# Optimization experiments

Measured on AMD Instinct MI355X. Metric: run time of the kernel, lower is better.

## Reference

```python
import jax, jax.numpy as jnp
import numpy as np

EMBED = 1024
HEADS = 16
HEAD = EMBED // HEADS
B, S = 8, 1024


def setup_inputs() -> dict:
    key = jax.random.key(0)
    ks = jax.random.split(key, 12)
    inp = {
        "values": jax.random.normal(ks[0], (B, S, EMBED), jnp.float32),
        "keys": jax.random.normal(ks[1], (B, S, EMBED), jnp.float32),
        "query": jax.random.normal(ks[2], (B, S, EMBED), jnp.float32),
        # causal mask broadcastable to [B, heads, q, k]
        "mask": jnp.broadcast_to(jnp.tril(jnp.ones((S, S), jnp.int32))[None, None], (B, 1, S, S)),
        "Wv": jax.random.normal(ks[3], (HEAD, HEAD), jnp.float32) / np.sqrt(HEAD),
        "bv": jnp.zeros((HEAD,), jnp.float32),
        "Wk": jax.random.normal(ks[4], (HEAD, HEAD), jnp.float32) / np.sqrt(HEAD),
        "bk": jnp.zeros((HEAD,), jnp.float32),
        "Wq": jax.random.normal(ks[5], (HEAD, HEAD), jnp.float32) / np.sqrt(HEAD),
        "bq": jnp.zeros((HEAD,), jnp.float32),
        "Wfc": jax.random.normal(ks[6], (EMBED, EMBED), jnp.float32) / np.sqrt(EMBED),
        "bfc": jnp.zeros((EMBED,), jnp.float32),
    }
    return inp


def reference(values, keys, query, mask, Wv, bv, Wk, bk, Wq, bq, Wfc, bfc):
    N, q_len = query.shape[0], query.shape[1]
    k_len, v_len = keys.shape[1], values.shape[1]
    # split heads: [N, S, H, D]
    v = values.reshape(N, v_len, HEADS, HEAD)
    k = keys.reshape(N, k_len, HEADS, HEAD)
    q = query.reshape(N, q_len, HEADS, HEAD)
    # per-head linear projections (torch Linear: x @ W.T + b)
    v = v @ Wv.T + bv
    k = k @ Wk.T + bk
    q = q @ Wq.T + bq
    # scores [N, H, q, k]
    scores = jnp.einsum('nqhz,nkhz->nhqk', q, k)
    scores = jnp.where(mask == 0, -jnp.inf, scores)
    # NOTE: original divides by sqrt(query_size) (sequence length), not head dim
    attn = jax.nn.softmax(scores / jnp.sqrt(jnp.float32(q_len)), axis=-1)
    out = jnp.einsum('nhqk,nkhz->nqhz', attn, v).reshape(N, q_len, HEADS * HEAD)
    return out @ Wfc.T + bfc
```

## Files before the change

kernel.cpp:

```cpp
#include <hip/hip_runtime.h>
#include <stdint.h>

typedef __attribute__((ext_vector_type(8))) short short8;
typedef __attribute__((ext_vector_type(4))) short short4v;
typedef __attribute__((ext_vector_type(4))) float floatx4;
typedef __attribute__((ext_vector_type(4))) unsigned short ushort4v;

#define HEADS 16
#define HEAD 64
#define SEQ 1024
#define BATCH 8

__device__ __forceinline__ unsigned short f2bf(float f) {
    union { float f; unsigned int u; } v; v.f = f;
    unsigned int r = v.u + 0x7FFFu + ((v.u >> 16) & 1u);
    return (unsigned short)(r >> 16);
}

__device__ __forceinline__ void gload_lds16(const void* g, void* l) {
    __builtin_amdgcn_global_load_lds((const __attribute__((address_space(1))) void*)g,
                                     (__attribute__((address_space(3))) void*)l, 16, 0, 0);
}

__global__ __launch_bounds__(256) void cvt_kernel(const float* __restrict__ in,
                                                  unsigned short* __restrict__ out) {
    int i = (blockIdx.x * 256 + threadIdx.x) * 4;
    float4 f = *(const float4*)(in + i);
    ushort4v v;
    v.x = f2bf(f.x); v.y = f2bf(f.y); v.z = f2bf(f.z); v.w = f2bf(f.w);
    *(ushort4v*)(out + i) = v;
}

__global__ __launch_bounds__(256, 3) void proj_kernel(
    const float* __restrict__ Vin, const float* __restrict__ Kin, const float* __restrict__ Qin,
    const float* __restrict__ Wv, const float* __restrict__ bv,
    const float* __restrict__ Wk, const float* __restrict__ bk,
    const float* __restrict__ Wq, const float* __restrict__ bq,
    unsigned short* __restrict__ q_ws, unsigned short* __restrict__ k_ws,
    unsigned short* __restrict__ v_ws)
{
    const int tid = threadIdx.x;
    const int tile = blockIdx.x;
    const int proj = blockIdx.y;

    const float* X; const float* W; const float* bias;
    if (proj == 0)      { X = Qin; W = Wq; bias = bq; }
    else if (proj == 1) { X = Kin; W = Wk; bias = bk; }
    else                { X = Vin; W = Wv; bias = bv; }

    __shared__ unsigned short sW[64 * 64];
    __shared__ unsigned short sE[4][16 * 72];

    const int wave = tid >> 6, lane = tid & 63;
    const int lq = lane & 15, quad = lane >> 4;
    const int m0 = tile * 16;
    const int b = m0 >> 10, s0 = m0 & 1023;
    const int h0 = blockIdx.z * 8 + wave * 2;

    const float qscale = 0.03125f * 1.44269504088896340736f;
    const float wscale = (proj == 0) ? qscale : 1.0f;

    float4 raw[2][4];
    {
        const float* xr = X + (size_t)(m0 + lq) * 1024 + h0 * 64 + quad * 8;
#pragma unroll
        for (int hh = 0; hh < 2; ++hh)
#pragma unroll
            for (int ks = 0; ks < 2; ++ks) {
                raw[hh][ks * 2 + 0] = *(const float4*)(xr + hh * 64 + ks * 32);
                raw[hh][ks * 2 + 1] = *(const float4*)(xr + hh * 64 + ks * 32 + 4);
            }
    }

    {
        int n = tid >> 2, c0 = (tid & 3) * 16;
        const float* wr = W + n * 64 + c0;
#pragma unroll
        for (int half = 0; half < 2; ++half) {
            float4 fa = *(const float4*)(wr + half * 8);
            float4 fb = *(const float4*)(wr + half * 8 + 4);
            short8 v;
            v[0] = (short)f2bf(fa.x * wscale); v[1] = (short)f2bf(fa.y * wscale);
            v[2] = (short)f2bf(fa.z * wscale); v[3] = (short)f2bf(fa.w * wscale);
            v[4] = (short)f2bf(fb.x * wscale); v[5] = (short)f2bf(fb.y * wscale);
            v[6] = (short)f2bf(fb.z * wscale); v[7] = (short)f2bf(fb.w * wscale);
            int chunk = ((c0 >> 3) + half) ^ (n & 7);
            *(short8*)&sW[n * 64 + chunk * 8] = v;
        }
    }

    float biasv[4];
#pragma unroll
    for (int nt = 0; nt < 4; ++nt) biasv[nt] = bias[nt * 16 + lq] * wscale;

    __syncthreads();

    short8 bfr[2][4];
#pragma unroll
    for (int ks = 0; ks < 2; ++ks)
#pragma unroll
        for (int nt = 0; nt < 4; ++nt) {
            int n = nt * 16 + lq;
            bfr[ks][nt] = *(const short8*)&sW[n * 64 + (((quad + 4 * ks) ^ (n & 7)) * 8)];
        }

    const floatx4 zero4 = {0.f, 0.f, 0.f, 0.f};

#pragma unroll
    for (int hh = 0; hh < 2; ++hh) {
        const int h = h0 + hh;

        short8 afr[2];
#pragma unroll
        for (int ks = 0; ks < 2; ++ks) {
            float4 f0 = raw[hh][ks * 2 + 0];
            float4 f1 = raw[hh][ks * 2 + 1];
            short8 a;
            a[0] = (short)f2bf(f0.x); a[1] = (short)f2bf(f0.y);
            a[2] = (short)f2bf(f0.z); a[3] = (short)f2bf(f0.w);
            a[4] = (short)f2bf(f1.x); a[5] = (short)f2bf(f1.y);
            a[6] = (short)f2bf(f1.z); a[7] = (short)f2bf(f1.w);
            afr[ks] = a;
        }

        floatx4 acc[4] = {zero4, zero4, zero4, zero4};
#pragma unroll
        for (int ks = 0; ks < 2; ++ks)
#pragma unroll
            for (int nt = 0; nt < 4; ++nt)
                acc[nt] = __builtin_amdgcn_mfma_f32_16x16x32_bf16(afr[ks], bfr[ks][nt], acc[nt], 0, 0, 0);

#pragma unroll
        for (int nt = 0; nt < 4; ++nt)
#pragma unroll
            for (int r = 0; r < 4; ++r)
                sE[wave][(quad * 4 + r) * 72 + nt * 16 + lq] = f2bf(acc[nt][r] + biasv[nt]);

        if (proj < 2) {
            unsigned short* dstb = (proj == 0 ? q_ws : k_ws);
            int row = lane >> 2, c = (lane & 3) * 16;
            const unsigned short* src = &sE[wave][row * 72 + c];
            unsigned short* dst = dstb + ((size_t)((b * 16 + h) * 1024 + s0 + row)) * 64 + c;
            *(short8*)dst = *(const short8*)src;
            *(short8*)(dst + 8) = *(const short8*)(src + 8);
        } else {
            int d = lane;
            short8 v[2];
#pragma unroll
            for (int g = 0; g < 2; ++g)
#pragma unroll
                for (int j = 0; j < 8; ++j)
                    v[g][j] = (short)sE[wave][(g * 8 + j) * 72 + d];
            unsigned short* dst = v_ws + ((size_t)((b * 16 + h) * 64 + d)) * 1024 + s0;
            *(short8*)dst = v[0];
            *(short8*)(dst + 8) = v[1];
        }
    }
}

__global__ __launch_bounds__(256, 3) void attn_kernel(
    const unsigned short* __restrict__ q_ws, const unsigned short* __restrict__ k_ws,
    const unsigned short* __restrict__ v_ws, unsigned short* __restrict__ attn_ws)
{
    const int bh = blockIdx.x;
    const int b = bh >> 4, h = bh & 15;
    const int tid = threadIdx.x;
    const int wave = tid >> 6, lane = tid & 63;
    const int lq = lane & 15, quad = lane >> 4;
    const int r8 = lane >> 3, ch = lane & 7;
    const int sw = ch ^ r8;

    __shared__ unsigned short sK[64 * 64];
    __shared__ unsigned short sV[64 * 64];
    __shared__ unsigned short sP[4][32 * 64];

    const size_t head_off = (size_t)bh * SEQ * HEAD;
    const unsigned short* qb = q_ws + head_off;
    const unsigned short* kb = k_ws + head_off;
    const unsigned short* vb = v_ws + head_off;

    short8 ones;
#pragma unroll
    for (int j = 0; j < 8; ++j) ones[j] = (short)0x3F80;

    const floatx4 zero4 = {0.f, 0.f, 0.f, 0.f};

    for (int pass = 0; pass < 2; ++pass) {
        const int qt = pass ? (7 - blockIdx.y) : blockIdx.y;
        const int q0 = qt * 128;
        const int q_lo = q0 + wave * 32;
        const int q_hi = q_lo + 31;
        const int nkt = 2 * qt + 2;

        short8 aq[2][2];
#pragma unroll
        for (int rg = 0; rg < 2; ++rg) {
            const unsigned short* qp = qb + (size_t)(q0 + wave * 32 + rg * 16 + lq) * 64 + quad * 8;
            aq[rg][0] = *(const short8*)qp;
            aq[rg][1] = *(const short8*)(qp + 32);
        }

        floatx4 o[2][4];
        floatx4 lacc[2] = {zero4, zero4};
#pragma unroll
        for (int rg = 0; rg < 2; ++rg)
#pragma unroll
            for (int nt = 0; nt < 4; ++nt) o[rg][nt] = zero4;

        for (int kt = 0; kt < nkt; ++kt) {
#pragma unroll
            for (int i = 0; i < 2; ++i) {
                int br = wave * 16 + i * 8;
                const char* gK = (const char*)(kb + (size_t)(kt * 64 + br + r8) * 64) + sw * 16;
                gload_lds16(gK, (char*)sK + br * 128);
                const char* gV = (const char*)(vb + (size_t)(br + r8) * 1024 + kt * 64) + sw * 16;
                gload_lds16(gV, (char*)sV + br * 128);
            }
            __syncthreads();

            const bool skip = (kt * 64 > q_hi);
            if (!skip) {
                const bool full = (kt * 64 + 63 <= q_lo);

                floatx4 sT[2][4];
#pragma unroll
                for (int rg = 0; rg < 2; ++rg)
#pragma unroll
                    for (int nt = 0; nt < 4; ++nt) sT[rg][nt] = zero4;
#pragma unroll
                for (int ks = 0; ks < 2; ++ks) {
#pragma unroll
                    for (int nt = 0; nt < 4; ++nt) {
                        short8 kf = *(const short8*)(sK + (nt * 16 + lq) * 64 +
                                                     (((quad + 4 * ks) ^ (lq & 7)) * 8));
                        sT[0][nt] = __builtin_amdgcn_mfma_f32_16x16x32_bf16(kf, aq[0][ks], sT[0][nt], 0, 0, 0);
                        sT[1][nt] = __builtin_amdgcn_mfma_f32_16x16x32_bf16(kf, aq[1][ks], sT[1][nt], 0, 0, 0);
                    }
                }

                unsigned short* wp = &sP[wave][0];
#pragma unroll
                for (int rg = 0; rg < 2; ++rg) {
                    int q = q_lo + rg * 16 + lq;
#pragma unroll
                    for (int nt = 0; nt < 4; ++nt) {
                        int kcol0 = kt * 64 + nt * 16 + quad * 4;
                        short4v pk;
#pragma unroll
                        for (int r = 0; r < 4; ++r) {
                            float p = __builtin_amdgcn_exp2f(sT[rg][nt][r]);
                            if (!full && (kcol0 + r > q)) p = 0.f;
                            pk[r] = (short)f2bf(p);
                        }
                        *(short4v*)&wp[(rg * 16 + lq) * 64 +
                                       (((nt * 2 + (quad >> 1)) ^ (lq & 7)) * 8) + (quad & 1) * 4] = pk;
                    }
                }

                short8 vf[4][2];
#pragma unroll
                for (int nt = 0; nt < 4; ++nt)
#pragma unroll
                    for (int ks = 0; ks < 2; ++ks)
                        vf[nt][ks] = *(const short8*)(sV + (nt * 16 + lq) * 64 +
                                                      (((quad + 4 * ks) ^ (lq & 7)) * 8));
#pragma unroll
                for (int rg = 0; rg < 2; ++rg) {
#pragma unroll
                    for (int ks = 0; ks < 2; ++ks) {
                        short8 pa = *(const short8*)&sP[wave][(rg * 16 + lq) * 64 +
                                     (((ks * 4 + quad) ^ (lq & 7)) * 8)];
                        lacc[rg] = __builtin_amdgcn_mfma_f32_16x16x32_bf16(pa, ones, lacc[rg], 0, 0, 0);
#pragma unroll
                        for (int nt = 0; nt < 4; ++nt)
                            o[rg][nt] = __builtin_amdgcn_mfma_f32_16x16x32_bf16(pa, vf[nt][ks], o[rg][nt], 0, 0, 0);
                    }
                }
            }
            __syncthreads();
        }

#pragma unroll
        for (int rg = 0; rg < 2; ++rg) {
            float inv[4];
#pragma unroll
            for (int r = 0; r < 4; ++r) inv[r] = 1.f / lacc[rg][r];
            const int srow_base = q0 + wave * 32 + rg * 16 + quad * 4;
#pragma unroll
            for (int nt = 0; nt < 4; ++nt) {
                int col = h * 64 + nt * 16 + lq;
#pragma unroll
                for (int r = 0; r < 4; ++r) {
                    attn_ws[((size_t)(b * SEQ + srow_base + r)) * 1024 + col] = f2bf(o[rg][nt][r] * inv[r]);
                }
            }
        }
    }
}

__global__ __launch_bounds__(256) void fc_kernel(
    const unsigned short* __restrict__ A, const unsigned short* __restrict__ Bw,
    const float* __restrict__ bias, float* __restrict__ out)
{
    const int nt0 = blockIdx.x * 128;
    const int mt0 = blockIdx.y * 128;
    const int tid = threadIdx.x;
    const int wave = tid >> 6, lane = tid & 63;
    const int lq = lane & 15, quad = lane >> 4;
    const int wm = (wave >> 1) * 64, wn = (wave & 1) * 64;

    __shared__ unsigned short sA[128 * 32];
    __shared__ unsigned short sB[128 * 32];

    const floatx4 zero4 = {0.f, 0.f, 0.f, 0.f};
    floatx4 acc[4][4];
#pragma unroll
    for (int i = 0; i < 4; ++i)
#pragma unroll
        for (int j = 0; j < 4; ++j) acc[i][j] = zero4;

    for (int kt = 0; kt < 32; ++kt) {
#pragma unroll
        for (int issue = 0; issue < 2; ++issue) {
            int off = (issue * 4 + wave) * 1024 + lane * 16;
            int row = off >> 6;
            int cb = off & 63;
            const char* ga = (const char*)A + (size_t)(mt0 + row) * 2048 + kt * 64 + cb;
            gload_lds16(ga, (char*)sA + (issue * 4 + wave) * 1024);
            const char* gb = (const char*)Bw + (size_t)(nt0 + row) * 2048 + kt * 64 + cb;
            gload_lds16(gb, (char*)sB + (issue * 4 + wave) * 1024);
        }
        __syncthreads();

        short8 af[4], bf[4];
#pragma unroll
        for (int i = 0; i < 4; ++i) {
            af[i] = *(const short8*)(sA + (wm + i * 16 + lq) * 32 + quad * 8);
            bf[i] = *(const short8*)(sB + (wn + i * 16 + lq) * 32 + quad * 8);
        }
#pragma unroll
        for (int mi = 0; mi < 4; ++mi)
#pragma unroll
            for (int ni = 0; ni < 4; ++ni)
                acc[mi][ni] = __builtin_amdgcn_mfma_f32_16x16x32_bf16(af[mi], bf[ni], acc[mi][ni], 0, 0, 0);
        __syncthreads();
    }

#pragma unroll
    for (int mi = 0; mi < 4; ++mi) {
#pragma unroll
        for (int ni = 0; ni < 4; ++ni) {
            int col = nt0 + wn + ni * 16 + lq;
            float bc = bias[col];
#pragma unroll
            for (int r = 0; r < 4; ++r) {
                int row = mt0 + wm + mi * 16 + quad * 4 + r;
                out[(size_t)row * 1024 + col] = acc[mi][ni][r] + bc;
            }
        }
    }
}

extern "C" void kernel_launch(void* const* d_in, const int* in_sizes, int n_in,
                              void* d_out, int out_size, void* d_ws, size_t ws_size,
                              hipStream_t stream)
{
    const float* values = (const float*)d_in[0];
    const float* keys   = (const float*)d_in[1];
    const float* query  = (const float*)d_in[2];
    const float* Wv  = (const float*)d_in[4];
    const float* bv  = (const float*)d_in[5];
    const float* Wk  = (const float*)d_in[6];
    const float* bk  = (const float*)d_in[7];
    const float* Wq  = (const float*)d_in[8];
    const float* bq  = (const float*)d_in[9];
    const float* Wfc = (const float*)d_in[10];
    const float* bfc = (const float*)d_in[11];
    float* out = (float*)d_out;

    char* ws = (char*)d_ws;
    unsigned short* q_ws    = (unsigned short*)(ws);
    unsigned short* k_ws    = (unsigned short*)(ws + (16u << 20));
    unsigned short* v_ws    = (unsigned short*)(ws + (32u << 20));
    unsigned short* attn_ws = (unsigned short*)(ws + (48u << 20));
    unsigned short* wfc_ws  = (unsigned short*)(ws + (64u << 20));

    cvt_kernel<<<dim3(1024), dim3(256), 0, stream>>>(Wfc, wfc_ws);
    proj_kernel<<<dim3(512, 3, 2), dim3(256), 0, stream>>>(
        values, keys, query, Wv, bv, Wk, bk, Wq, bq, q_ws, k_ws, v_ws);
    attn_kernel<<<dim3(128, 4), dim3(256), 0, stream>>>(q_ws, k_ws, v_ws, attn_ws);
    fc_kernel<<<dim3(8, 64), dim3(256), 0, stream>>>(attn_ws, wfc_ws, bfc, out);
}
```

Measured before the change: 253.2 us.

## Double-buffer attention and FC tiles, restage projection through LDS, split attention grid

The projection kernel now loads a full 16x1024 row tile into LDS with coalesced loads and handles all 16 heads per block, keeping weights in registers and dropping the z-split. The attention kernel double-buffers K/V tiles in LDS so the next tile's load overlaps compute. It also launches 8 query-tile blocks per head instead of pairing tiles, which gives up the manual load balancing in exchange for more blocks. The FC GEMM double-buffers its A/B tiles and drops one barrier per k-step. Larger LDS footprints may reduce occupancy.

```diff
diff --git a/kernel.cpp b/kernel.cpp
--- a/kernel.cpp
+++ b/kernel.cpp
@@ -48,117 +48,115 @@
     else if (proj == 1) { X = Kin; W = Wk; bias = bk; }
     else                { X = Vin; W = Wv; bias = bv; }
 
-    __shared__ unsigned short sW[64 * 64];
-    __shared__ unsigned short sE[4][16 * 72];
+    __shared__ unsigned short sX[16 * 1024];
 
     const int wave = tid >> 6, lane = tid & 63;
     const int lq = lane & 15, quad = lane >> 4;
     const int m0 = tile * 16;
     const int b = m0 >> 10, s0 = m0 & 1023;
-    const int h0 = blockIdx.z * 8 + wave * 2;
 
     const float qscale = 0.03125f * 1.44269504088896340736f;
     const float wscale = (proj == 0) ? qscale : 1.0f;
 
-    float4 raw[2][4];
-    {
-        const float* xr = X + (size_t)(m0 + lq) * 1024 + h0 * 64 + quad * 8;
-#pragma unroll
-        for (int hh = 0; hh < 2; ++hh)
-#pragma unroll
-            for (int ks = 0; ks < 2; ++ks) {
-                raw[hh][ks * 2 + 0] = *(const float4*)(xr + hh * 64 + ks * 32);
-                raw[hh][ks * 2 + 1] = *(const float4*)(xr + hh * 64 + ks * 32 + 4);
-            }
-    }
-
-    {
-        int n = tid >> 2, c0 = (tid & 3) * 16;
-        const float* wr = W + n * 64 + c0;
-#pragma unroll
-        for (int half = 0; half < 2; ++half) {
-            float4 fa = *(const float4*)(wr + half * 8);
-            float4 fb = *(const float4*)(wr + half * 8 + 4);
+    const float* Xb = X + (size_t)m0 * 1024;
+    float4 xr[8][2];
+#pragma unroll
+    for (int i = 0; i < 8; ++i) {
+        int c = i * 256 + tid;
+        xr[i][0] = *(const float4*)(Xb + (size_t)c * 8);
+        xr[i][1] = *(const float4*)(Xb + (size_t)c * 8 + 4);
+    }
+
+    short8 bfr[2][4];
+#pragma unroll
+    for (int ks = 0; ks < 2; ++ks)
+#pragma unroll
+        for (int nt = 0; nt < 4; ++nt) {
+            const float* wp2 = W + (nt * 16 + lq) * 64 + ks * 32 + quad * 8;
+            float4 f0 = *(const float4*)(wp2);
+            float4 f1 = *(const float4*)(wp2 + 4);
             short8 v;
-            v[0] = (short)f2bf(fa.x * wscale); v[1] = (short)f2bf(fa.y * wscale);
-            v[2] = (short)f2bf(fa.z * wscale); v[3] = (short)f2bf(fa.w * wscale);
-            v[4] = (short)f2bf(fb.x * wscale); v[5] = (short)f2bf(fb.y * wscale);
-            v[6] = (short)f2bf(fb.z * wscale); v[7] = (short)f2bf(fb.w * wscale);
-            int chunk = ((c0 >> 3) + half) ^ (n & 7);
-            *(short8*)&sW[n * 64 + chunk * 8] = v;
-        }
-    }
+            v[0] = (short)f2bf(f0.x * wscale); v[1] = (short)f2bf(f0.y * wscale);
+            v[2] = (short)f2bf(f0.z * wscale); v[3] = (short)f2bf(f0.w * wscale);
+            v[4] = (short)f2bf(f1.x * wscale); v[5] = (short)f2bf(f1.y * wscale);
+            v[6] = (short)f2bf(f1.z * wscale); v[7] = (short)f2bf(f1.w * wscale);
+            bfr[ks][nt] = v;
+        }
 
     float biasv[4];
 #pragma unroll
     for (int nt = 0; nt < 4; ++nt) biasv[nt] = bias[nt * 16 + lq] * wscale;
 
+#pragma unroll
+    for (int i = 0; i < 8; ++i) {
+        int c = i * 256 + tid;
+        int row = c >> 7, cc = c & 127;
+        int ccs = cc ^ (row & 7);
+        short8 v;
+        float4 f0 = xr[i][0], f1 = xr[i][1];
+        v[0] = (short)f2bf(f0.x); v[1] = (short)f2bf(f0.y);
+        v[2] = (short)f2bf(f0.z); v[3] = (short)f2bf(f0.w);
+        v[4] = (short)f2bf(f1.x); v[5] = (short)f2bf(f1.y);
+        v[6] = (short)f2bf(f1.z); v[7] = (short)f2bf(f1.w);
+        *(short8*)&sX[row * 1024 + ccs * 8] = v;
+    }
     __syncthreads();
 
-    short8 bfr[2][4];
-#pragma unroll
-    for (int ks = 0; ks < 2; ++ks)
-#pragma unroll
-        for (int nt = 0; nt < 4; ++nt) {
-            int n = nt * 16 + lq;
-            bfr[ks][nt] = *(const short8*)&sW[n * 64 + (((quad + 4 * ks) ^ (n & 7)) * 8)];
-        }
+    short8 afr[4][2];
+#pragma unroll
+    for (int hh = 0; hh < 4; ++hh) {
+        int h = wave * 4 + hh;
+#pragma unroll
+        for (int ks = 0; ks < 2; ++ks) {
+            int cc = h * 8 + ks * 4 + quad;
+            afr[hh][ks] = *(const short8*)&sX[lq * 1024 + (cc ^ (lq & 7)) * 8];
+        }
+    }
+    __syncthreads();
+
+    unsigned short* sE = sX + wave * 1152;
 
     const floatx4 zero4 = {0.f, 0.f, 0.f, 0.f};
 
 #pragma unroll
-    for (int hh = 0; hh < 2; ++hh) {
-        const int h = h0 + hh;
-
-        short8 afr[2];
-#pragma unroll
-        for (int ks = 0; ks < 2; ++ks) {
-            float4 f0 = raw[hh][ks * 2 + 0];
-            float4 f1 = raw[hh][ks * 2 + 1];
-            short8 a;
-            a[0] = (short)f2bf(f0.x); a[1] = (short)f2bf(f0.y);
-            a[2] = (short)f2bf(f0.z); a[3] = (short)f2bf(f0.w);
-            a[4] = (short)f2bf(f1.x); a[5] = (short)f2bf(f1.y);
-            a[6] = (short)f2bf(f1.z); a[7] = (short)f2bf(f1.w);
-            afr[ks] = a;
-        }
+    for (int hh = 0; hh < 4; ++hh) {
+        const int h = wave * 4 + hh;
 
         floatx4 acc[4] = {zero4, zero4, zero4, zero4};
 #pragma unroll
         for (int ks = 0; ks < 2; ++ks)
 #pragma unroll
             for (int nt = 0; nt < 4; ++nt)
-                acc[nt] = __builtin_amdgcn_mfma_f32_16x16x32_bf16(afr[ks], bfr[ks][nt], acc[nt], 0, 0, 0);
+                acc[nt] = __builtin_amdgcn_mfma_f32_16x16x32_bf16(afr[hh][ks], bfr[ks][nt], acc[nt], 0, 0, 0);
 
 #pragma unroll
         for (int nt = 0; nt < 4; ++nt)
 #pragma unroll
             for (int r = 0; r < 4; ++r)
-                sE[wave][(quad * 4 + r) * 72 + nt * 16 + lq] = f2bf(acc[nt][r] + biasv[nt]);
+                sE[(quad * 4 + r) * 72 + nt * 16 + lq] = f2bf(acc[nt][r] + biasv[nt]);
 
         if (proj < 2) {
             unsigned short* dstb = (proj == 0 ? q_ws : k_ws);
             int row = lane >> 2, c = (lane & 3) * 16;
-            const unsigned short* src = &sE[wave][row * 72 + c];
+            const unsigned short* src = &sE[row * 72 + c];
             unsigned short* dst = dstb + ((size_t)((b * 16 + h) * 1024 + s0 + row)) * 64 + c;
             *(short8*)dst = *(const short8*)src;
             *(short8*)(dst + 8) = *(const short8*)(src + 8);
         } else {
             int d = lane;
-            short8 v[2];
-#pragma unroll
-            for (int g = 0; g < 2; ++g)
-#pragma unroll
-                for (int j = 0; j < 8; ++j)
-                    v[g][j] = (short)sE[wave][(g * 8 + j) * 72 + d];
+            short8 v0, v1;
+#pragma unroll
+            for (int j = 0; j < 8; ++j) v0[j] = (short)sE[j * 72 + d];
+#pragma unroll
+            for (int j = 0; j < 8; ++j) v1[j] = (short)sE[(8 + j) * 72 + d];
             unsigned short* dst = v_ws + ((size_t)((b * 16 + h) * 64 + d)) * 1024 + s0;
-            *(short8*)dst = v[0];
-            *(short8*)(dst + 8) = v[1];
-        }
-    }
-}
-
-__global__ __launch_bounds__(256, 3) void attn_kernel(
+            *(short8*)dst = v0;
+            *(short8*)(dst + 8) = v1;
+        }
+    }
+}
+
+__global__ __launch_bounds__(256, 4) void attn_kernel(
     const unsigned short* __restrict__ q_ws, const unsigned short* __restrict__ k_ws,
     const unsigned short* __restrict__ v_ws, unsigned short* __restrict__ attn_ws)
 {
@@ -170,135 +168,143 @@
     const int r8 = lane >> 3, ch = lane & 7;
     const int sw = ch ^ r8;
 
-    __shared__ unsigned short sK[64 * 64];
-    __shared__ unsigned short sV[64 * 64];
-    __shared__ unsigned short sP[4][32 * 64];
+    __shared__ char sKV[2][16384];
+    __shared__ unsigned short sP[4][1024];
 
     const size_t head_off = (size_t)bh * SEQ * HEAD;
     const unsigned short* qb = q_ws + head_off;
     const unsigned short* kb = k_ws + head_off;
     const unsigned short* vb = v_ws + head_off;
 
+    const int qt = 7 - blockIdx.y;
+    const int q0 = qt * 128;
+    const int q_lo = q0 + wave * 32;
+    const int q_hi = q_lo + 31;
+    const int nkt = 2 * qt + 2;
+
     short8 ones;
 #pragma unroll
     for (int j = 0; j < 8; ++j) ones[j] = (short)0x3F80;
 
+    short8 aq[2][2];
+#pragma unroll
+    for (int rg = 0; rg < 2; ++rg) {
+        const unsigned short* qp = qb + (size_t)(q0 + wave * 32 + rg * 16 + lq) * 64 + quad * 8;
+        aq[rg][0] = *(const short8*)qp;
+        aq[rg][1] = *(const short8*)(qp + 32);
+    }
+
     const floatx4 zero4 = {0.f, 0.f, 0.f, 0.f};
-
-    for (int pass = 0; pass < 2; ++pass) {
-        const int qt = pass ? (7 - blockIdx.y) : blockIdx.y;
-        const int q0 = qt * 128;
-        const int q_lo = q0 + wave * 32;
-        const int q_hi = q_lo + 31;
-        const int nkt = 2 * qt + 2;
-
-        short8 aq[2][2];
-#pragma unroll
-        for (int rg = 0; rg < 2; ++rg) {
-            const unsigned short* qp = qb + (size_t)(q0 + wave * 32 + rg * 16 + lq) * 64 + quad * 8;
-            aq[rg][0] = *(const short8*)qp;
-            aq[rg][1] = *(const short8*)(qp + 32);
-        }
-
-        floatx4 o[2][4];
-        floatx4 lacc[2] = {zero4, zero4};
-#pragma unroll
-        for (int rg = 0; rg < 2; ++rg)
-#pragma unroll
-            for (int nt = 0; nt < 4; ++nt) o[rg][nt] = zero4;
-
-        for (int kt = 0; kt < nkt; ++kt) {
+    floatx4 o[2][4];
+    floatx4 lacc[2] = {zero4, zero4};
+#pragma unroll
+    for (int rg = 0; rg < 2; ++rg)
+#pragma unroll
+        for (int nt = 0; nt < 4; ++nt) o[rg][nt] = zero4;
+
+    {
+        char* dst = sKV[0];
+#pragma unroll
+        for (int i = 0; i < 2; ++i) {
+            int br = wave * 16 + i * 8;
+            const char* gK = (const char*)(kb + (size_t)(0 * 64 + br + r8) * 64) + sw * 16;
+            gload_lds16(gK, dst + br * 128);
+            const char* gV = (const char*)(vb + (size_t)(br + r8) * 1024 + 0 * 64) + sw * 16;
+            gload_lds16(gV, dst + 8192 + br * 128);
+        }
+    }
+
+    for (int kt = 0; kt < nkt; ++kt) {
+        __syncthreads();
+
+        if (kt + 1 < nkt) {
+            char* dst = sKV[(kt + 1) & 1];
 #pragma unroll
             for (int i = 0; i < 2; ++i) {
                 int br = wave * 16 + i * 8;
-                const char* gK = (const char*)(kb + (size_t)(kt * 64 + br + r8) * 64) + sw * 16;
-                gload_lds16(gK, (char*)sK + br * 128);
-                const char* gV = (const char*)(vb + (size_t)(br + r8) * 1024 + kt * 64) + sw * 16;
-                gload_lds16(gV, (char*)sV + br * 128);
-            }
-            __syncthreads();
-
-            const bool skip = (kt * 64 > q_hi);
-            if (!skip) {
-                const bool full = (kt * 64 + 63 <= q_lo);
-
-                floatx4 sT[2][4];
-#pragma unroll
-                for (int rg = 0; rg < 2; ++rg)
-#pragma unroll
-                    for (int nt = 0; nt < 4; ++nt) sT[rg][nt] = zero4;
-#pragma unroll
-                for (int ks = 0; ks < 2; ++ks) {
-#pragma unroll
-                    for (int nt = 0; nt < 4; ++nt) {
-                        short8 kf = *(const short8*)(sK + (nt * 16 + lq) * 64 +
-                                                     (((quad + 4 * ks) ^ (lq & 7)) * 8));
-                        sT[0][nt] = __builtin_amdgcn_mfma_f32_16x16x32_bf16(kf, aq[0][ks], sT[0][nt], 0, 0, 0);
-                        sT[1][nt] = __builtin_amdgcn_mfma_f32_16x16x32_bf16(kf, aq[1][ks], sT[1][nt], 0, 0, 0);
-                    }
+                const char* gK = (const char*)(kb + (size_t)((kt + 1) * 64 + br + r8) * 64) + sw * 16;
+                gload_lds16(gK, dst + br * 128);
+                const char* gV = (const char*)(vb + (size_t)(br + r8) * 1024 + (kt + 1) * 64) + sw * 16;
+                gload_lds16(gV, dst + 8192 + br * 128);
+            }
+        }
+
+        if (kt * 64 > q_hi) continue;
+        const bool full = (kt * 64 + 63 <= q_lo);
+
+        const unsigned short* sK = (const unsigned short*)sKV[kt & 1];
+        const unsigned short* sV = sK + 4096;
+
+        floatx4 sT[2][4];
+#pragma unroll
+        for (int rg = 0; rg < 2; ++rg)
+#pragma unroll
+            for (int nt = 0; nt < 4; ++nt) sT[rg][nt] = zero4;
+#pragma unroll
+        for (int ks = 0; ks < 2; ++ks) {
+#pragma unroll
+            for (int nt = 0; nt < 4; ++nt) {
+                short8 kf = *(const short8*)(sK + (nt * 16 + lq) * 64 +
+                                             (((quad + 4 * ks) ^ (lq & 7)) * 8));
+                sT[0][nt] = __builtin_amdgcn_mfma_f32_16x16x32_bf16(kf, aq[0][ks], sT[0][nt], 0, 0, 0);
+                sT[1][nt] = __builtin_amdgcn_mfma_f32_16x16x32_bf16(kf, aq[1][ks], sT[1][nt], 0, 0, 0);
+            }
+        }
+
+        short8 vf[4][2];
+#pragma unroll
+        for (int nt = 0; nt < 4; ++nt)
+#pragma unroll
+            for (int ks = 0; ks < 2; ++ks)
+                vf[nt][ks] = *(const short8*)(sV + (nt * 16 + lq) * 64 +
+                                              (((quad + 4 * ks) ^ (lq & 7)) * 8));
+
+        unsigned short* wp = &sP[wave][0];
+#pragma unroll
+        for (int rg = 0; rg < 2; ++rg) {
+            int q = q_lo + rg * 16 + lq;
+#pragma unroll
+            for (int nt = 0; nt < 4; ++nt) {
+                int kcol0 = kt * 64 + nt * 16 + quad * 4;
+                short4v pk;
+#pragma unroll
+                for (int r = 0; r < 4; ++r) {
+                    float p = __builtin_amdgcn_exp2f(sT[rg][nt][r]);
+                    if (!full && (kcol0 + r > q)) p = 0.f;
+                    pk[r] = (short)f2bf(p);
                 }
-
-                unsigned short* wp = &sP[wave][0];
-#pragma unroll
-                for (int rg = 0; rg < 2; ++rg) {
-                    int q = q_lo + rg * 16 + lq;
-#pragma unroll
-                    for (int nt = 0; nt < 4; ++nt) {
-                        int kcol0 = kt * 64 + nt * 16 + quad * 4;
-                        short4v pk;
-#pragma unroll
-                        for (int r = 0; r < 4; ++r) {
-                            float p = __builtin_amdgcn_exp2f(sT[rg][nt][r]);
-                            if (!full && (kcol0 + r > q)) p = 0.f;
-                            pk[r] = (short)f2bf(p);
-                        }
-                        *(short4v*)&wp[(rg * 16 + lq) * 64 +
-                                       (((nt * 2 + (quad >> 1)) ^ (lq & 7)) * 8) + (quad & 1) * 4] = pk;
-                    }
-                }
-
-                short8 vf[4][2];
+                *(short4v*)&wp[lq * 64 +
+                               (((nt * 2 + (quad >> 1)) ^ (lq & 7)) * 8) + (quad & 1) * 4] = pk;
+            }
+#pragma unroll
+            for (int ks = 0; ks < 2; ++ks) {
+                short8 pa = *(const short8*)&wp[lq * 64 + (((ks * 4 + quad) ^ (lq & 7)) * 8)];
+                lacc[rg] = __builtin_amdgcn_mfma_f32_16x16x32_bf16(pa, ones, lacc[rg], 0, 0, 0);
 #pragma unroll
                 for (int nt = 0; nt < 4; ++nt)
-#pragma unroll
-                    for (int ks = 0; ks < 2; ++ks)
-                        vf[nt][ks] = *(const short8*)(sV + (nt * 16 + lq) * 64 +
-                                                      (((quad + 4 * ks) ^ (lq & 7)) * 8));
-#pragma unroll
-                for (int rg = 0; rg < 2; ++rg) {
-#pragma unroll
-                    for (int ks = 0; ks < 2; ++ks) {
-                        short8 pa = *(const short8*)&sP[wave][(rg * 16 + lq) * 64 +
-                                     (((ks * 4 + quad) ^ (lq & 7)) * 8)];
-                        lacc[rg] = __builtin_amdgcn_mfma_f32_16x16x32_bf16(pa, ones, lacc[rg], 0, 0, 0);
-#pragma unroll
-                        for (int nt = 0; nt < 4; ++nt)
-                            o[rg][nt] = __builtin_amdgcn_mfma_f32_16x16x32_bf16(pa, vf[nt][ks], o[rg][nt], 0, 0, 0);
-                    }
-                }
-            }
-            __syncthreads();
-        }
-
-#pragma unroll
-        for (int rg = 0; rg < 2; ++rg) {
-            float inv[4];
-#pragma unroll
-            for (int r = 0; r < 4; ++r) inv[r] = 1.f / lacc[rg][r];
-            const int srow_base = q0 + wave * 32 + rg * 16 + quad * 4;
-#pragma unroll
-            for (int nt = 0; nt < 4; ++nt) {
-                int col = h * 64 + nt * 16 + lq;
-#pragma unroll
-                for (int r = 0; r < 4; ++r) {
-                    attn_ws[((size_t)(b * SEQ + srow_base + r)) * 1024 + col] = f2bf(o[rg][nt][r] * inv[r]);
-                }
-            }
-        }
-    }
-}
-
-__global__ __launch_bounds__(256) void fc_kernel(
+                    o[rg][nt] = __builtin_amdgcn_mfma_f32_16x16x32_bf16(pa, vf[nt][ks], o[rg][nt], 0, 0, 0);
+            }
+        }
+    }
+
+#pragma unroll
+    for (int rg = 0; rg < 2; ++rg) {
+        float inv[4];
+#pragma unroll
+        for (int r = 0; r < 4; ++r) inv[r] = 1.f / lacc[rg][r];
+        const int srow_base = q0 + wave * 32 + rg * 16 + quad * 4;
+#pragma unroll
+        for (int nt = 0; nt < 4; ++nt) {
+            int col = h * 64 + nt * 16 + lq;
+#pragma unroll
+            for (int r = 0; r < 4; ++r) {
+                attn_ws[((size_t)(b * SEQ + srow_base + r)) * 1024 + col] = f2bf(o[rg][nt][r] * inv[r]);
+            }
+        }
+    }
+}
+
+__global__ __launch_bounds__(256, 2) void fc_kernel(
     const unsigned short* __restrict__ A, const unsigned short* __restrict__ Bw,
     const float* __restrict__ bias, float* __restrict__ out)
 {
@@ -309,8 +315,7 @@
     const int lq = lane & 15, quad = lane >> 4;
     const int wm = (wave >> 1) * 64, wn = (wave & 1) * 64;
 
-    __shared__ unsigned short sA[128 * 32];
-    __shared__ unsigned short sB[128 * 32];
+    __shared__ char sAB[2][16384];
 
     const floatx4 zero4 = {0.f, 0.f, 0.f, 0.f};
     floatx4 acc[4][4];
@@ -319,18 +324,32 @@
 #pragma unroll
         for (int j = 0; j < 4; ++j) acc[i][j] = zero4;
 
+#pragma unroll
+    for (int issue = 0; issue < 2; ++issue) {
+        int off = (issue * 4 + wave) * 1024 + lane * 16;
+        int row = off >> 6, cb = off & 63;
+        gload_lds16((const char*)A + (size_t)(mt0 + row) * 2048 + cb, sAB[0] + (issue * 4 + wave) * 1024);
+        gload_lds16((const char*)Bw + (size_t)(nt0 + row) * 2048 + cb, sAB[0] + 8192 + (issue * 4 + wave) * 1024);
+    }
+
     for (int kt = 0; kt < 32; ++kt) {
-#pragma unroll
-        for (int issue = 0; issue < 2; ++issue) {
-            int off = (issue * 4 + wave) * 1024 + lane * 16;
-            int row = off >> 6;
-            int cb = off & 63;
-            const char* ga = (const char*)A + (size_t)(mt0 + row) * 2048 + kt * 64 + cb;
-            gload_lds16(ga, (char*)sA + (issue * 4 + wave) * 1024);
-            const char* gb = (const char*)Bw + (size_t)(nt0 + row) * 2048 + kt * 64 + cb;
-            gload_lds16(gb, (char*)sB + (issue * 4 + wave) * 1024);
-        }
         __syncthreads();
+
+        if (kt < 31) {
+            char* dst = sAB[(kt + 1) & 1];
+#pragma unroll
+            for (int issue = 0; issue < 2; ++issue) {
+                int off = (issue * 4 + wave) * 1024 + lane * 16;
+                int row = off >> 6, cb = off & 63;
+                gload_lds16((const char*)A + (size_t)(mt0 + row) * 2048 + (kt + 1) * 64 + cb,
+                            dst + (issue * 4 + wave) * 1024);
+                gload_lds16((const char*)Bw + (size_t)(nt0 + row) * 2048 + (kt + 1) * 64 + cb,
+                            dst + 8192 + (issue * 4 + wave) * 1024);
+            }
+        }
+
+        const unsigned short* sA = (const unsigned short*)sAB[kt & 1];
+        const unsigned short* sB = sA + 4096;
 
         short8 af[4], bf[4];
 #pragma unroll
@@ -343,7 +362,6 @@
 #pragma unroll
             for (int ni = 0; ni < 4; ++ni)
                 acc[mi][ni] = __builtin_amdgcn_mfma_f32_16x16x32_bf16(af[mi], bf[ni], acc[mi][ni], 0, 0, 0);
-        __syncthreads();
     }
 
 #pragma unroll
@@ -386,8 +404,8 @@
     unsigned short* wfc_ws  = (unsigned short*)(ws + (64u << 20));
 
     cvt_kernel<<<dim3(1024), dim3(256), 0, stream>>>(Wfc, wfc_ws);
-    proj_kernel<<<dim3(512, 3, 2), dim3(256), 0, stream>>>(
+    proj_kernel<<<dim3(512, 3), dim3(256), 0, stream>>>(
         values, keys, query, Wv, bv, Wk, bk, Wq, bq, q_ws, k_ws, v_ws);
-    attn_kernel<<<dim3(128, 4), dim3(256), 0, stream>>>(q_ws, k_ws, v_ws, attn_ws);
+    attn_kernel<<<dim3(128, 8), dim3(256), 0, stream>>>(q_ws, k_ws, v_ws, attn_ws);
     fc_kernel<<<dim3(8, 64), dim3(256), 0, stream>>>(attn_ws, wfc_ws, bfc, out);
 }
```

New measurement: 292.6 us. 15.6% more time.
